# Kernel tuning notes

Measured on AMD Instinct MI355X. Metric: run time of the kernel, lower is better.

The kernel has to match this reference:

```python
import jax, jax.numpy as jnp
import numpy as np

LEAKY_SLOPE = 0.01  # torch F.leaky_relu default
COS_EPS = 1e-8      # torch F.cosine_similarity default eps


def _gc(pre, cur, adj, W):
    # GraphConvolution.forward
    pre_w = pre @ W            # [N, d]
    cur_w = cur @ W            # [M, d]
    new_pre = adj @ cur_w      # [N, d]
    new_cur = adj.T @ pre_w    # [M, d]
    new_pre = jnp.where(new_pre >= 0, new_pre, LEAKY_SLOPE * new_pre)
    new_cur = jnp.where(new_cur >= 0, new_cur, LEAKY_SLOPE * new_cur)
    return new_pre, new_cur


def _cos_sim(pre, cur):
    # Fused pairwise cosine similarity: matches torch F.cosine_similarity per pair
    dots = pre @ cur.T                         # [N, M]
    n_pre = jnp.linalg.norm(pre, axis=1)       # [N]
    n_cur = jnp.linalg.norm(cur, axis=1)       # [M]
    denom = jnp.maximum(n_pre[:, None] * n_cur[None, :], COS_EPS)
    return dots / denom


def setup_inputs() -> dict:
    key = jax.random.key(0)
    k1, k2, k3, k4, k5 = jax.random.split(key, 5)
    N, d = 8192, 128
    stdv = 1.0 / np.sqrt(d)
    pre = jax.random.normal(k1, (N, d), dtype=jnp.float32)
    cur = jax.random.normal(k2, (N, d), dtype=jnp.float32)
    adj = jax.random.uniform(k3, (N, N), dtype=jnp.float32)
    W1 = jax.random.uniform(k4, (d, d), dtype=jnp.float32, minval=-stdv, maxval=stdv)
    W2 = jax.random.uniform(k5, (d, d), dtype=jnp.float32, minval=-stdv, maxval=stdv)
    return {"pre": pre, "cur": cur, "adj": adj, "W1": W1, "W2": W2}


def reference(pre, cur, adj, W1, W2):
    pre1, cur1 = _gc(pre, cur, adj, W1)
    adj1 = _cos_sim(pre1, cur1)
    pre2, cur2 = _gc(pre1, cur1, adj1, W2)
    adj2 = _cos_sim(pre2, cur2)
    return adj2
```

## Files before the change

kernel.cpp:

```cpp
#include <hip/hip_runtime.h>


#define NN 8192
#define DD 128

typedef __bf16 bf16x8 __attribute__((ext_vector_type(8)));
typedef float f32x4 __attribute__((ext_vector_type(4)));

static __device__ __forceinline__ float4 ldg4(const float* p) {
    return *reinterpret_cast<const float4*>(p);
}

static __device__ __forceinline__ unsigned f2bf2(float lo, float hi) {
    __bf16 a = (__bf16)lo, b = (__bf16)hi;
    unsigned short ua = __builtin_bit_cast(unsigned short, a);
    unsigned short ub = __builtin_bit_cast(unsigned short, b);
    return (unsigned)ua | ((unsigned)ub << 16);
}

static __device__ __forceinline__ int swz16(int row) {
    return (((row & 7) ^ ((row >> 3) & 7)) << 4);
}

template<int AMODE>
__global__ __launch_bounds__(256, 2)
void mfma_tn(const void* __restrict__ Aptr, int lda,
             const unsigned short* __restrict__ BTa,
             const unsigned short* __restrict__ BTb, int ldbt,
             float* __restrict__ C, int ldc,
             int ksplit, int zstride)
{
    __shared__ uint4 smem4[2048];
    char* smem = (char*)smem4;
    char* smA = smem;
    char* smB = smem + 16384;

    const int t    = threadIdx.x;
    const int l    = t & 63;
    const int w    = t >> 6;
    const int wr   = (w >> 1) * 64;
    const int wc   = (w & 1) * 64;
    const int lrow = l & 15;
    const int lhi  = l >> 4;
    const int i0   = blockIdx.x * 128;
    const int j0   = blockIdx.y * 128;
    const int z    = blockIdx.z;
    const bool second = (AMODE == 3) && (z >= 8);
    const unsigned short* BT = second ? BTb : BTa;
    const int kbase = (AMODE == 3) ? (z & 7) * ksplit : 0;
    C += (size_t)z * (size_t)zstride;

    const int srow = t >> 3;
    const int skg  = t & 7;

    f32x4 acc[4][4];
    #pragma unroll
    for (int r = 0; r < 4; ++r)
        #pragma unroll
        for (int q = 0; q < 4; ++q)
            #pragma unroll
            for (int e = 0; e < 4; ++e) acc[r][q][e] = 0.0f;

    for (int k0 = 0; k0 < ksplit; k0 += 64) {
        const int kk = kbase + k0;

        if (AMODE == 3 && second) {
            const int u  = t & 31;
            const int r8 = t >> 5;
            const float* gA = (const float*)Aptr;
            float rv[8][4];
            #pragma unroll
            for (int e = 0; e < 8; ++e) {
                float4 v = ldg4(&gA[(size_t)(kk + r8 * 8 + e) * lda + i0 + u * 4]);
                rv[e][0] = v.x; rv[e][1] = v.y; rv[e][2] = v.z; rv[e][3] = v.w;
            }
            #pragma unroll
            for (int j = 0; j < 4; ++j) {
                const int c = u * 4 + j;
                uint4 wv;
                wv.x = f2bf2(rv[0][j], rv[1][j]);
                wv.y = f2bf2(rv[2][j], rv[3][j]);
                wv.z = f2bf2(rv[4][j], rv[5][j]);
                wv.w = f2bf2(rv[6][j], rv[7][j]);
                *reinterpret_cast<uint4*>(smA + c * 128 + ((r8 << 4) ^ swz16(c))) = wv;
            }
        } else {
            #pragma unroll
            for (int it = 0; it < 4; ++it) {
                const int row = it * 32 + srow;
                const int dst = row * 128 + ((skg << 4) ^ swz16(row));
                if constexpr (AMODE == 3) {
                    const float* g = (const float*)Aptr + (size_t)(i0 + row) * lda + kk + skg * 8;
                    float4 f0 = ldg4(g), f1 = ldg4(g + 4);
                    uint4 wv;
                    wv.x = f2bf2(f0.x, f0.y);
                    wv.y = f2bf2(f0.z, f0.w);
                    wv.z = f2bf2(f1.x, f1.y);
                    wv.w = f2bf2(f1.z, f1.w);
                    *reinterpret_cast<uint4*>(smA + dst) = wv;
                } else {
                    const unsigned short* g = (const unsigned short*)Aptr + (size_t)(i0 + row) * lda + kk + skg * 8;
                    *reinterpret_cast<uint4*>(smA + dst) = *reinterpret_cast<const uint4*>(g);
                }
            }
        }

        #pragma unroll
        for (int it = 0; it < 4; ++it) {
            const int row = it * 32 + srow;
            const int dst = row * 128 + ((skg << 4) ^ swz16(row));
            const unsigned short* gb = BT + (size_t)(j0 + row) * ldbt + kk + skg * 8;
            *reinterpret_cast<uint4*>(smB + dst) = *reinterpret_cast<const uint4*>(gb);
        }
        __syncthreads();

        #pragma unroll
        for (int s = 0; s < 2; ++s) {
            bf16x8 af[4], bq[4];
            #pragma unroll
            for (int r = 0; r < 4; ++r) {
                const int row = wr + r * 16 + lrow;
                af[r] = *reinterpret_cast<const bf16x8*>(
                    smA + row * 128 + ((s * 64 + lhi * 16) ^ swz16(row)));
            }
            #pragma unroll
            for (int q = 0; q < 4; ++q) {
                const int col = wc + q * 16 + lrow;
                bq[q] = *reinterpret_cast<const bf16x8*>(
                    smB + col * 128 + ((s * 64 + lhi * 16) ^ swz16(col)));
            }
            #pragma unroll
            for (int r = 0; r < 4; ++r)
                #pragma unroll
                for (int q = 0; q < 4; ++q)
                    acc[r][q] = __builtin_amdgcn_mfma_f32_16x16x32_bf16(af[r], bq[q], acc[r][q], 0, 0, 0);
        }
        __syncthreads();
    }

    float* sC = (float*)smem;
    #pragma unroll
    for (int h = 0; h < 2; ++h) {
        if ((w & 1) == h) {
            #pragma unroll
            for (int r = 0; r < 4; ++r)
                #pragma unroll
                for (int q = 0; q < 4; ++q)
                    #pragma unroll
                    for (int i = 0; i < 4; ++i)
                        sC[(wr + r * 16 + lhi * 4 + i) * 64 + q * 16 + lrow] = acc[r][q][i];
        }
        __syncthreads();
        #pragma unroll
        for (int it = 0; it < 8; ++it) {
            const int idx = it * 256 + t;
            const int row = idx >> 4;
            const int c4  = (idx & 15) << 2;
            float4 v = *reinterpret_cast<const float4*>(&sC[row * 64 + c4]);
            *reinterpret_cast<float4*>(&C[(size_t)(i0 + row) * ldc + j0 + h * 64 + c4]) = v;
        }
        __syncthreads();
    }
}

__global__ __launch_bounds__(256, 2)
void gemm_w1t(const float* __restrict__ pre, const float* __restrict__ cur,
              const float* __restrict__ W1,
              unsigned short* __restrict__ pwT, unsigned short* __restrict__ cwT)
{
    __shared__ float sA[32][68];
    __shared__ float sB[64][128];

    const int t  = threadIdx.x;
    const int ct = t & 31;
    const int rt = t >> 5;
    const int bx = blockIdx.x;
    const bool isCur = bx >= 256;
    const float* A = isCur ? cur : pre;
    unsigned short* XT = isCur ? cwT : pwT;
    const int i0 = (bx & 255) * 32;

    float4 acc[4];
    #pragma unroll
    for (int r = 0; r < 4; ++r) { acc[r].x = 0.f; acc[r].y = 0.f; acc[r].z = 0.f; acc[r].w = 0.f; }

    for (int k0 = 0; k0 < DD; k0 += 64) {
        #pragma unroll
        for (int f = 0; f < 2; ++f) {
            const int row = (t >> 4) + 16 * f;
            const int kk4 = (t & 15) << 2;
            *reinterpret_cast<float4*>(&sA[row][kk4]) =
                ldg4(&A[(size_t)(i0 + row) * DD + k0 + kk4]);
        }
        #pragma unroll
        for (int f = 0; f < 8; ++f) {
            const int idx = f * 256 + t;
            const int kk  = idx >> 5;
            const int c4  = (idx & 31) << 2;
            *reinterpret_cast<float4*>(&sB[kk][c4]) =
                ldg4(&W1[(size_t)(k0 + kk) * DD + c4]);
        }
        __syncthreads();
        #pragma unroll 4
        for (int kk = 0; kk < 64; kk += 4) {
            float4 a[4], b[4];
            #pragma unroll
            for (int r = 0; r < 4; ++r)
                a[r] = *reinterpret_cast<const float4*>(&sA[rt * 4 + r][kk]);
            #pragma unroll
            for (int q = 0; q < 4; ++q)
                b[q] = *reinterpret_cast<const float4*>(&sB[kk + q][ct * 4]);
            #pragma unroll
            for (int r = 0; r < 4; ++r) {
                acc[r].x += a[r].x * b[0].x; acc[r].y += a[r].x * b[0].y;
                acc[r].z += a[r].x * b[0].z; acc[r].w += a[r].x * b[0].w;
                acc[r].x += a[r].y * b[1].x; acc[r].y += a[r].y * b[1].y;
                acc[r].z += a[r].y * b[1].z; acc[r].w += a[r].y * b[1].w;
                acc[r].x += a[r].z * b[2].x; acc[r].y += a[r].z * b[2].y;
                acc[r].z += a[r].z * b[2].z; acc[r].w += a[r].z * b[2].w;
                acc[r].x += a[r].w * b[3].x; acc[r].y += a[r].w * b[3].y;
                acc[r].z += a[r].w * b[3].z; acc[r].w += a[r].w * b[3].w;
            }
        }
        __syncthreads();
    }

    float* sC = &sB[0][0];
    #pragma unroll
    for (int r = 0; r < 4; ++r)
        *reinterpret_cast<float4*>(&sC[(rt * 4 + r) * 128 + ct * 4]) = acc[r];
    __syncthreads();

    const int n = t & 127;
    const int g = t >> 7;
    #pragma unroll
    for (int c = 0; c < 2; ++c) {
        const int ii = (2 * g + c) * 8;
        uint4 wv;
        wv.x = f2bf2(sC[(ii + 0) * 128 + n], sC[(ii + 1) * 128 + n]);
        wv.y = f2bf2(sC[(ii + 2) * 128 + n], sC[(ii + 3) * 128 + n]);
        wv.z = f2bf2(sC[(ii + 4) * 128 + n], sC[(ii + 5) * 128 + n]);
        wv.w = f2bf2(sC[(ii + 6) * 128 + n], sC[(ii + 7) * 128 + n]);
        *reinterpret_cast<uint4*>(&XT[(size_t)n * NN + i0 + ii]) = wv;
    }
}

__global__ __launch_bounds__(128)
void rln(const float* __restrict__ kparts, float* __restrict__ Xbase,
         float* __restrict__ invbase)
{
    const int i = blockIdx.x;
    const int y = blockIdx.y;
    const int t = threadIdx.x;
    const float* part = kparts + (size_t)(1 - y) * 8 * (NN * DD);
    float* X = Xbase + (size_t)y * (NN * DD);
    float* inv_n = invbase + y * NN;

    float s = 0.f;
    #pragma unroll
    for (int z = 0; z < 8; ++z)
        s += part[(size_t)z * (NN * DD) + (size_t)i * DD + t];
    float y_ = (s >= 0.f) ? s : 0.01f * s;
    X[(size_t)i * DD + t] = y_;
    float n = y_ * y_;
    #pragma unroll
    for (int o = 32; o > 0; o >>= 1) n += __shfl_down(n, o);
    __shared__ float p[2];
    if ((t & 63) == 0) p[t >> 6] = n;
    __syncthreads();
    if (t == 0) inv_n[i] = 1.0f / sqrtf(p[0] + p[1]);
}

template<bool TRANSA, bool SCALEK, int EPI>
__global__ __launch_bounds__(256, 2)
void gemm32(const float* __restrict__ A, int lda,
            const float* __restrict__ B, int ldb,
            float* __restrict__ C, unsigned short* __restrict__ Cb,
            int ksplit_len, int zstride,
            const float* __restrict__ kscale,
            const float* __restrict__ rscale,
            int ystA, int ystB, int ystC, int ystS)
{
    __shared__ float sA[32][68];
    __shared__ float sB[64][128];

    const int t  = threadIdx.x;
    const int ct = t & 31;
    const int rt = t >> 5;
    const int i0 = blockIdx.x * 32;
    const int side = blockIdx.y;
    const int kgbase = blockIdx.z * ksplit_len;

    A += (ptrdiff_t)side * ystA;
    B += (ptrdiff_t)side * ystB;
    if constexpr (EPI == 0)
        C += (ptrdiff_t)side * ystC + (size_t)blockIdx.z * (size_t)zstride;
    if constexpr (EPI == 3)
        Cb += (ptrdiff_t)side * ystC;
    if constexpr (SCALEK) kscale += (ptrdiff_t)side * ystS;
    if constexpr (EPI == 3) rscale += (ptrdiff_t)side * ystS;

    float4 acc[4];
    #pragma unroll
    for (int r = 0; r < 4; ++r) { acc[r].x = 0.f; acc[r].y = 0.f; acc[r].z = 0.f; acc[r].w = 0.f; }

    for (int k0 = 0; k0 < ksplit_len; k0 += 64) {
        const int kg = kgbase + k0;
        if (!TRANSA) {
            #pragma unroll
            for (int f = 0; f < 2; ++f) {
                const int row = (t >> 4) + 16 * f;
                const int kk4 = (t & 15) << 2;
                *reinterpret_cast<float4*>(&sA[row][kk4]) =
                    ldg4(&A[(size_t)(i0 + row) * lda + kg + kk4]);
            }
        } else {
            #pragma unroll
            for (int f = 0; f < 2; ++f) {
                const int kk = (t >> 3) + 32 * f;
                const int r4 = (t & 7) << 2;
                float4 v = ldg4(&A[(size_t)(kg + kk) * lda + i0 + r4]);
                if (SCALEK) {
                    const float s = kscale[kg + kk];
                    v.x *= s; v.y *= s; v.z *= s; v.w *= s;
                }
                sA[r4 + 0][kk] = v.x; sA[r4 + 1][kk] = v.y;
                sA[r4 + 2][kk] = v.z; sA[r4 + 3][kk] = v.w;
            }
        }
        #pragma unroll
        for (int f = 0; f < 8; ++f) {
            const int idx = f * 256 + t;
            const int kk  = idx >> 5;
            const int c4  = (idx & 31) << 2;
            *reinterpret_cast<float4*>(&sB[kk][c4]) =
                ldg4(&B[(size_t)(kg + kk) * ldb + c4]);
        }
        __syncthreads();
        #pragma unroll 4
        for (int kk = 0; kk < 64; kk += 4) {
            float4 a[4], b[4];
            #pragma unroll
            for (int r = 0; r < 4; ++r)
                a[r] = *reinterpret_cast<const float4*>(&sA[rt * 4 + r][kk]);
            #pragma unroll
            for (int q = 0; q < 4; ++q)
                b[q] = *reinterpret_cast<const float4*>(&sB[kk + q][ct * 4]);
            #pragma unroll
            for (int r = 0; r < 4; ++r) {
                acc[r].x += a[r].x * b[0].x; acc[r].y += a[r].x * b[0].y;
                acc[r].z += a[r].x * b[0].z; acc[r].w += a[r].x * b[0].w;
                acc[r].x += a[r].y * b[1].x; acc[r].y += a[r].y * b[1].y;
                acc[r].z += a[r].y * b[1].z; acc[r].w += a[r].y * b[1].w;
                acc[r].x += a[r].z * b[2].x; acc[r].y += a[r].z * b[2].y;
                acc[r].z += a[r].z * b[2].z; acc[r].w += a[r].z * b[2].w;
                acc[r].x += a[r].w * b[3].x; acc[r].y += a[r].w * b[3].y;
                acc[r].z += a[r].w * b[3].z; acc[r].w += a[r].w * b[3].w;
            }
        }
        __syncthreads();
    }

    #pragma unroll
    for (int r = 0; r < 4; ++r) {
        const int rg = i0 + rt * 4 + r;
        if constexpr (EPI == 3) {
            const float s = rscale[rg];
            float y0 = acc[r].x * s, y1 = acc[r].y * s,
                  y2 = acc[r].z * s, y3 = acc[r].w * s;
            y0 = (y0 >= 0.f) ? y0 : 0.01f * y0;
            y1 = (y1 >= 0.f) ? y1 : 0.01f * y1;
            y2 = (y2 >= 0.f) ? y2 : 0.01f * y2;
            y3 = (y3 >= 0.f) ? y3 : 0.01f * y3;
            float ss = y0 * y0 + y1 * y1 + y2 * y2 + y3 * y3;
            #pragma unroll
            for (int m = 16; m > 0; m >>= 1) ss += __shfl_xor(ss, m);
            const float invn = rsqrtf(ss);
            uint2 wv;
            wv.x = f2bf2(y0 * invn, y1 * invn);
            wv.y = f2bf2(y2 * invn, y3 * invn);
            *reinterpret_cast<uint2*>(&Cb[(size_t)rg * DD + ct * 4]) = wv;
        } else {
            *reinterpret_cast<float4*>(&C[(size_t)rg * DD + ct * 4]) = acc[r];
        }
    }
}

__global__ __launch_bounds__(256)
void reduce_mcmp(const float* __restrict__ part, float* __restrict__ out)
{
    const int y = blockIdx.y;
    const int i = blockIdx.x * 256 + threadIdx.x;
    part += (size_t)y * 32 * 16384;
    out  += (size_t)y * 16384;
    float a = 0.f;
    #pragma unroll
    for (int z = 0; z < 32; ++z) a += part[(size_t)z * 16384 + i];
    out[i] = a;
}

extern "C" void kernel_launch(void* const* d_in, const int* in_sizes, int n_in,
                              void* d_out, int out_size, void* d_ws, size_t ws_size,
                              hipStream_t stream)
{
    const float* pre = (const float*)d_in[0];
    const float* cur = (const float*)d_in[1];
    const float* adj = (const float*)d_in[2];
    const float* W1  = (const float*)d_in[3];
    const float* W2  = (const float*)d_in[4];
    float* out = (float*)d_out;
    float* ws  = (float*)d_ws;

    const size_t M1 = (size_t)NN * DD;

    float* cwpw2 = ws + 0 * M1;
    float* c1    = ws + 2 * M1;
    unsigned short* c2n_b = (unsigned short*)(ws + 4 * M1);
    unsigned short* p2n_b = c2n_b + M1;
    unsigned short* cwT_b = (unsigned short*)(ws + 5 * M1);
    unsigned short* pwT_b = cwT_b + M1;
    float* bparts = ws + 6 * M1;
    float* mcmp   = ws + 7 * M1;
    float* inc1   = mcmp + 32768;
    float* kparts = ws + 8 * M1;

    gemm_w1t<<<dim3(512,1,1),256,0,stream>>>(pre, cur, W1, pwT_b, cwT_b);

    mfma_tn<3><<<dim3(64,1,16),256,0,stream>>>(adj, NN, cwT_b, pwT_b, NN,
                                               kparts, DD, NN/8, (int)M1);

    rln<<<dim3(NN,2,1),128,0,stream>>>(kparts, c1, inc1);

    gemm32<false,false,0><<<dim3(512,1,1),256,0,stream>>>(
        c1, DD, W2, DD, cwpw2, (unsigned short*)nullptr,
        DD, 0, nullptr, nullptr, 0,0,0,0);

    gemm32<true,true,0><<<dim3(4,2,32),256,0,stream>>>(
        c1, DD, cwpw2, DD, bparts, (unsigned short*)nullptr,
        256, 16384, inc1, nullptr,
        (int)M1, (int)M1, 32*16384, NN);

    reduce_mcmp<<<dim3(64,2,1),256,0,stream>>>(bparts, mcmp);

    gemm32<false,false,3><<<dim3(256,2,1),256,0,stream>>>(
        c1, DD, mcmp + 16384, DD, (float*)nullptr, c2n_b,
        DD, 0, nullptr, inc1,
        (int)M1, -16384, (int)M1, NN);

    mfma_tn<0><<<dim3(64,64,1),256,0,stream>>>(p2n_b, DD, c2n_b, c2n_b, DD,
                                               out, NN, DD, 0);
}
```

Measured before the change: 286.7 us.

## Double-buffer mfma_tn shared memory with register prefetch and halve split-K

The bf16 MFMA GEMM kernel now loads the next K-tile from global memory into registers while it runs MFMAs on the current tile, using two shared-memory buffers and one barrier per iteration. The split-K factor for the first adjacency GEMM drops from 8 to 4, which halves the partial buffers written and summed by rln. The epilogue pads the staging stride to 68 to avoid LDS bank conflicts and uses nontemporal stores for AMODE 0. Shared memory doubles to 64KB per block and register pressure rises, which may limit occupancy, and the grid shrinks to 512 blocks.

```diff
diff --git a/kernel.cpp b/kernel.cpp
--- a/kernel.cpp
+++ b/kernel.cpp
@@ -17,6 +17,8 @@
     unsigned short ub = __builtin_bit_cast(unsigned short, b);
     return (unsigned)ua | ((unsigned)ub << 16);
 }
+
+#define FCOMP(v, j) ((j) == 0 ? (v).x : (j) == 1 ? (v).y : (j) == 2 ? (v).z : (v).w)
 
 static __device__ __forceinline__ int swz16(int row) {
     return (((row & 7) ^ ((row >> 3) & 7)) << 4);
@@ -30,10 +32,8 @@
              float* __restrict__ C, int ldc,
              int ksplit, int zstride)
 {
-    __shared__ uint4 smem4[2048];
+    __shared__ uint4 smem4[4096];
     char* smem = (char*)smem4;
-    char* smA = smem;
-    char* smB = smem + 16384;
 
     const int t    = threadIdx.x;
     const int l    = t & 63;
@@ -45,13 +45,15 @@
     const int i0   = blockIdx.x * 128;
     const int j0   = blockIdx.y * 128;
     const int z    = blockIdx.z;
-    const bool second = (AMODE == 3) && (z >= 8);
+    const bool second = (AMODE == 3) && (z >= 4);
     const unsigned short* BT = second ? BTb : BTa;
-    const int kbase = (AMODE == 3) ? (z & 7) * ksplit : 0;
+    const int kbase = (AMODE == 3) ? (z & 3) * ksplit : 0;
     C += (size_t)z * (size_t)zstride;
 
     const int srow = t >> 3;
     const int skg  = t & 7;
+    const int u    = t & 31;
+    const int r8   = t >> 5;
 
     f32x4 acc[4][4];
     #pragma unroll
@@ -61,59 +63,79 @@
             #pragma unroll
             for (int e = 0; e < 4; ++e) acc[r][q][e] = 0.0f;
 
-    for (int k0 = 0; k0 < ksplit; k0 += 64) {
-        const int kk = kbase + k0;
-
+    float4 fa[8];
+    uint4  ua[4];
+    uint4  ub[4];
+
+    auto LOAD = [&](int kk) {
         if (AMODE == 3 && second) {
-            const int u  = t & 31;
-            const int r8 = t >> 5;
             const float* gA = (const float*)Aptr;
-            float rv[8][4];
-            #pragma unroll
-            for (int e = 0; e < 8; ++e) {
-                float4 v = ldg4(&gA[(size_t)(kk + r8 * 8 + e) * lda + i0 + u * 4]);
-                rv[e][0] = v.x; rv[e][1] = v.y; rv[e][2] = v.z; rv[e][3] = v.w;
-            }
+            #pragma unroll
+            for (int e = 0; e < 8; ++e)
+                fa[e] = ldg4(&gA[(size_t)(kk + r8 * 8 + e) * lda + i0 + u * 4]);
+        } else if (AMODE == 3) {
+            #pragma unroll
+            for (int it = 0; it < 4; ++it) {
+                const float* g = (const float*)Aptr + (size_t)(i0 + it * 32 + srow) * lda + kk + skg * 8;
+                fa[2 * it]     = ldg4(g);
+                fa[2 * it + 1] = ldg4(g + 4);
+            }
+        } else {
+            #pragma unroll
+            for (int it = 0; it < 4; ++it) {
+                const unsigned short* g = (const unsigned short*)Aptr + (size_t)(i0 + it * 32 + srow) * lda + kk + skg * 8;
+                ua[it] = *reinterpret_cast<const uint4*>(g);
+            }
+        }
+        #pragma unroll
+        for (int it = 0; it < 4; ++it) {
+            const unsigned short* gb = BT + (size_t)(j0 + it * 32 + srow) * ldbt + kk + skg * 8;
+            ub[it] = *reinterpret_cast<const uint4*>(gb);
+        }
+    };
+
+    auto WRITE = [&](int buf) {
+        char* smA = smem + buf * 32768;
+        char* smB = smA + 16384;
+        if (AMODE == 3 && second) {
             #pragma unroll
             for (int j = 0; j < 4; ++j) {
                 const int c = u * 4 + j;
                 uint4 wv;
-                wv.x = f2bf2(rv[0][j], rv[1][j]);
-                wv.y = f2bf2(rv[2][j], rv[3][j]);
-                wv.z = f2bf2(rv[4][j], rv[5][j]);
-                wv.w = f2bf2(rv[6][j], rv[7][j]);
+                wv.x = f2bf2(FCOMP(fa[0], j), FCOMP(fa[1], j));
+                wv.y = f2bf2(FCOMP(fa[2], j), FCOMP(fa[3], j));
+                wv.z = f2bf2(FCOMP(fa[4], j), FCOMP(fa[5], j));
+                wv.w = f2bf2(FCOMP(fa[6], j), FCOMP(fa[7], j));
                 *reinterpret_cast<uint4*>(smA + c * 128 + ((r8 << 4) ^ swz16(c))) = wv;
             }
-        } else {
+        } else if (AMODE == 3) {
             #pragma unroll
             for (int it = 0; it < 4; ++it) {
                 const int row = it * 32 + srow;
-                const int dst = row * 128 + ((skg << 4) ^ swz16(row));
-                if constexpr (AMODE == 3) {
-                    const float* g = (const float*)Aptr + (size_t)(i0 + row) * lda + kk + skg * 8;
-                    float4 f0 = ldg4(g), f1 = ldg4(g + 4);
-                    uint4 wv;
-                    wv.x = f2bf2(f0.x, f0.y);
-                    wv.y = f2bf2(f0.z, f0.w);
-                    wv.z = f2bf2(f1.x, f1.y);
-                    wv.w = f2bf2(f1.z, f1.w);
-                    *reinterpret_cast<uint4*>(smA + dst) = wv;
-                } else {
-                    const unsigned short* g = (const unsigned short*)Aptr + (size_t)(i0 + row) * lda + kk + skg * 8;
-                    *reinterpret_cast<uint4*>(smA + dst) = *reinterpret_cast<const uint4*>(g);
-                }
-            }
-        }
-
+                uint4 wv;
+                wv.x = f2bf2(fa[2 * it].x, fa[2 * it].y);
+                wv.y = f2bf2(fa[2 * it].z, fa[2 * it].w);
+                wv.z = f2bf2(fa[2 * it + 1].x, fa[2 * it + 1].y);
+                wv.w = f2bf2(fa[2 * it + 1].z, fa[2 * it + 1].w);
+                *reinterpret_cast<uint4*>(smA + row * 128 + ((skg << 4) ^ swz16(row))) = wv;
+            }
+        } else {
+            #pragma unroll
+            for (int it = 0; it < 4; ++it) {
+                const int row = it * 32 + srow;
+                *reinterpret_cast<uint4*>(smA + row * 128 + ((skg << 4) ^ swz16(row))) = ua[it];
+            }
+        }
         #pragma unroll
         for (int it = 0; it < 4; ++it) {
             const int row = it * 32 + srow;
-            const int dst = row * 128 + ((skg << 4) ^ swz16(row));
-            const unsigned short* gb = BT + (size_t)(j0 + row) * ldbt + kk + skg * 8;
-            *reinterpret_cast<uint4*>(smB + dst) = *reinterpret_cast<const uint4*>(gb);
-        }
-        __syncthreads();
-
+            *reinterpret_cast<uint4*>(smB + row * 128 + ((skg << 4) ^ swz16(row))) = ub[it];
+        }
+    };
+
+    auto MFMA_STEP = [&](int buf) {
+        char* smA = smem + buf * 32768;
+        char* smB = smA + 16384;
         #pragma unroll
         for (int s = 0; s < 2; ++s) {
             bf16x8 af[4], bq[4];
@@ -135,6 +157,17 @@
                 for (int q = 0; q < 4; ++q)
                     acc[r][q] = __builtin_amdgcn_mfma_f32_16x16x32_bf16(af[r], bq[q], acc[r][q], 0, 0, 0);
         }
+    };
+
+    const int nt = ksplit >> 6;
+    LOAD(kbase);
+    WRITE(0);
+    __syncthreads();
+    for (int tt = 0; tt < nt; ++tt) {
+        const int cur = tt & 1;
+        if (tt + 1 < nt) LOAD(kbase + (tt + 1) * 64);
+        MFMA_STEP(cur);
+        if (tt + 1 < nt) WRITE(cur ^ 1);
         __syncthreads();
     }
 
@@ -148,7 +181,7 @@
                 for (int q = 0; q < 4; ++q)
                     #pragma unroll
                     for (int i = 0; i < 4; ++i)
-                        sC[(wr + r * 16 + lhi * 4 + i) * 64 + q * 16 + lrow] = acc[r][q][i];
+                        sC[(wr + r * 16 + lhi * 4 + i) * 68 + q * 16 + lrow] = acc[r][q][i];
         }
         __syncthreads();
         #pragma unroll
@@ -156,8 +189,12 @@
             const int idx = it * 256 + t;
             const int row = idx >> 4;
             const int c4  = (idx & 15) << 2;
-            float4 v = *reinterpret_cast<const float4*>(&sC[row * 64 + c4]);
-            *reinterpret_cast<float4*>(&C[(size_t)(i0 + row) * ldc + j0 + h * 64 + c4]) = v;
+            f32x4 v = *reinterpret_cast<const f32x4*>(&sC[row * 68 + c4]);
+            float* dst = &C[(size_t)(i0 + row) * ldc + j0 + h * 64 + c4];
+            if constexpr (AMODE == 0)
+                __builtin_nontemporal_store(v, reinterpret_cast<f32x4*>(dst));
+            else
+                *reinterpret_cast<f32x4*>(dst) = v;
         }
         __syncthreads();
     }
@@ -252,13 +289,13 @@
     const int i = blockIdx.x;
     const int y = blockIdx.y;
     const int t = threadIdx.x;
-    const float* part = kparts + (size_t)(1 - y) * 8 * (NN * DD);
+    const float* part = kparts + (size_t)(1 - y) * 4 * (NN * DD);
     float* X = Xbase + (size_t)y * (NN * DD);
     float* inv_n = invbase + y * NN;
 
     float s = 0.f;
     #pragma unroll
-    for (int z = 0; z < 8; ++z)
+    for (int z = 0; z < 4; ++z)
         s += part[(size_t)z * (NN * DD) + (size_t)i * DD + t];
     float y_ = (s >= 0.f) ? s : 0.01f * s;
     X[(size_t)i * DD + t] = y_;
@@ -426,8 +463,8 @@
 
     gemm_w1t<<<dim3(512,1,1),256,0,stream>>>(pre, cur, W1, pwT_b, cwT_b);
 
-    mfma_tn<3><<<dim3(64,1,16),256,0,stream>>>(adj, NN, cwT_b, pwT_b, NN,
-                                               kparts, DD, NN/8, (int)M1);
+    mfma_tn<3><<<dim3(64,1,8),256,0,stream>>>(adj, NN, cwT_b, pwT_b, NN,
+                                              kparts, DD, NN/4, (int)M1);
 
     rln<<<dim3(NN,2,1),128,0,stream>>>(kparts, c1, inc1);
 
```

Result: slower. 294.2 us (+2.6%).

## Split MFMA GEMM into adj and output kernels with 128-deep K tiles

Applied to the files above, without the earlier changes.

Replaces the templated mfma_tn kernel with two specialised kernels. mfma_adj stages 128-wide K chunks per iteration (64KB LDS), halving the number of barriers per K and issuing more loads in flight. mfma_out loads the full K=128 panel once with a single sync and writes the accumulators straight to global memory instead of staging them through LDS. The larger LDS footprint may limit occupancy to one block per CU despite launch_bounds(256,2), and the direct output stores are less coalesced.

```diff
diff --git a/kernel.cpp b/kernel.cpp
--- a/kernel.cpp
+++ b/kernel.cpp
@@ -18,22 +18,154 @@
     return (unsigned)ua | ((unsigned)ub << 16);
 }
 
+#define FC(v, j) ((j) == 0 ? (v).x : (j) == 1 ? (v).y : (j) == 2 ? (v).z : (v).w)
+
+#define PRAGU _Pragma("unroll")
+
 static __device__ __forceinline__ int swz16(int row) {
     return (((row & 7) ^ ((row >> 3) & 7)) << 4);
 }
-
-template<int AMODE>
+static __device__ __forceinline__ int lslot(int row, int slot) {
+    return ((slot & 8) << 4) | (((slot & 7) << 4) ^ swz16(row));
+}
+
 __global__ __launch_bounds__(256, 2)
-void mfma_tn(const void* __restrict__ Aptr, int lda,
-             const unsigned short* __restrict__ BTa,
-             const unsigned short* __restrict__ BTb, int ldbt,
-             float* __restrict__ C, int ldc,
-             int ksplit, int zstride)
-{
-    __shared__ uint4 smem4[2048];
-    char* smem = (char*)smem4;
+void mfma_adj(const float* __restrict__ adj,
+              const unsigned short* __restrict__ BTa,
+              const unsigned short* __restrict__ BTb,
+              float* __restrict__ C, int ksplit, int zstride)
+{
+    __shared__ alignas(16) char smem[65536];
     char* smA = smem;
-    char* smB = smem + 16384;
+    char* smB = smem + 32768;
+
+    const int t    = threadIdx.x;
+    const int l    = t & 63;
+    const int w    = t >> 6;
+    const int wr   = (w >> 1) * 64;
+    const int wc   = (w & 1) * 64;
+    const int lrow = l & 15;
+    const int lhi  = l >> 4;
+    const int i0   = blockIdx.x * 128;
+    const int z    = blockIdx.z;
+    const bool second = z >= 8;
+    const unsigned short* BT = second ? BTb : BTa;
+    const int kbase = (z & 7) * ksplit;
+    C += (size_t)z * (size_t)zstride;
+
+    const int srow = t >> 3;
+    const int skg  = t & 7;
+    const int u    = t & 31;
+    const int r8   = t >> 5;
+
+    f32x4 acc[4][4];
+    PRAGU
+    for (int r = 0; r < 4; ++r)
+        PRAGU
+        for (int q = 0; q < 4; ++q)
+            PRAGU
+            for (int e = 0; e < 4; ++e) acc[r][q][e] = 0.0f;
+
+    const int nt = ksplit >> 7;
+    for (int tc = 0; tc < nt; ++tc) {
+        const int kk = kbase + tc * 128;
+
+        PRAGU
+        for (int h = 0; h < 2; ++h) {
+            const int kh = kk + h * 64;
+            if (second) {
+                float4 rv[8];
+                PRAGU
+                for (int e = 0; e < 8; ++e)
+                    rv[e] = ldg4(&adj[(size_t)(kh + r8 * 8 + e) * NN + i0 + u * 4]);
+                PRAGU
+                for (int j = 0; j < 4; ++j) {
+                    const int c = u * 4 + j;
+                    uint4 wv;
+                    wv.x = f2bf2(FC(rv[0], j), FC(rv[1], j));
+                    wv.y = f2bf2(FC(rv[2], j), FC(rv[3], j));
+                    wv.z = f2bf2(FC(rv[4], j), FC(rv[5], j));
+                    wv.w = f2bf2(FC(rv[6], j), FC(rv[7], j));
+                    *reinterpret_cast<uint4*>(smA + c * 256 + lslot(c, h * 8 + r8)) = wv;
+                }
+            } else {
+                PRAGU
+                for (int it = 0; it < 4; ++it) {
+                    const int row = it * 32 + srow;
+                    const float* g = adj + (size_t)(i0 + row) * NN + kh + skg * 8;
+                    float4 f0 = ldg4(g), f1 = ldg4(g + 4);
+                    uint4 wv;
+                    wv.x = f2bf2(f0.x, f0.y);
+                    wv.y = f2bf2(f0.z, f0.w);
+                    wv.z = f2bf2(f1.x, f1.y);
+                    wv.w = f2bf2(f1.z, f1.w);
+                    *reinterpret_cast<uint4*>(smA + row * 256 + lslot(row, h * 8 + skg)) = wv;
+                }
+            }
+            PRAGU
+            for (int it = 0; it < 4; ++it) {
+                const int n = it * 32 + srow;
+                *reinterpret_cast<uint4*>(smB + n * 256 + lslot(n, h * 8 + skg)) =
+                    *reinterpret_cast<const uint4*>(BT + (size_t)n * NN + kh + skg * 8);
+            }
+        }
+        __syncthreads();
+
+        PRAGU
+        for (int s = 0; s < 4; ++s) {
+            bf16x8 af[4], bq[4];
+            PRAGU
+            for (int r = 0; r < 4; ++r) {
+                const int row = wr + r * 16 + lrow;
+                af[r] = *reinterpret_cast<const bf16x8*>(smA + row * 256 + lslot(row, s * 4 + lhi));
+            }
+            PRAGU
+            for (int q = 0; q < 4; ++q) {
+                const int col = wc + q * 16 + lrow;
+                bq[q] = *reinterpret_cast<const bf16x8*>(smB + col * 256 + lslot(col, s * 4 + lhi));
+            }
+            PRAGU
+            for (int r = 0; r < 4; ++r)
+                PRAGU
+                for (int q = 0; q < 4; ++q)
+                    acc[r][q] = __builtin_amdgcn_mfma_f32_16x16x32_bf16(af[r], bq[q], acc[r][q], 0, 0, 0);
+        }
+        __syncthreads();
+    }
+
+    float* sC = (float*)smem;
+    PRAGU
+    for (int h = 0; h < 2; ++h) {
+        if ((w & 1) == h) {
+            PRAGU
+            for (int r = 0; r < 4; ++r)
+                PRAGU
+                for (int q = 0; q < 4; ++q)
+                    PRAGU
+                    for (int i = 0; i < 4; ++i)
+                        sC[(wr + r * 16 + lhi * 4 + i) * 68 + q * 16 + lrow] = acc[r][q][i];
+        }
+        __syncthreads();
+        PRAGU
+        for (int it = 0; it < 8; ++it) {
+            const int idx = it * 256 + t;
+            const int row = idx >> 4;
+            const int c4  = (idx & 15) << 2;
+            f32x4 v = *reinterpret_cast<const f32x4*>(&sC[row * 68 + c4]);
+            *reinterpret_cast<f32x4*>(&C[(size_t)(i0 + row) * DD + h * 64 + c4]) = v;
+        }
+        __syncthreads();
+    }
+}
+
+__global__ __launch_bounds__(256, 2)
+void mfma_out(const unsigned short* __restrict__ A,
+              const unsigned short* __restrict__ BT,
+              float* __restrict__ C)
+{
+    __shared__ alignas(16) char smem[65536];
+    char* smA = smem;
+    char* smB = smem + 32768;
 
     const int t    = threadIdx.x;
     const int l    = t & 63;
@@ -44,123 +176,57 @@
     const int lhi  = l >> 4;
     const int i0   = blockIdx.x * 128;
     const int j0   = blockIdx.y * 128;
-    const int z    = blockIdx.z;
-    const bool second = (AMODE == 3) && (z >= 8);
-    const unsigned short* BT = second ? BTb : BTa;
-    const int kbase = (AMODE == 3) ? (z & 7) * ksplit : 0;
-    C += (size_t)z * (size_t)zstride;
-
-    const int srow = t >> 3;
-    const int skg  = t & 7;
+    const int s16  = t >> 4;
+    const int slot = t & 15;
 
     f32x4 acc[4][4];
-    #pragma unroll
+    PRAGU
     for (int r = 0; r < 4; ++r)
-        #pragma unroll
+        PRAGU
         for (int q = 0; q < 4; ++q)
-            #pragma unroll
+            PRAGU
             for (int e = 0; e < 4; ++e) acc[r][q][e] = 0.0f;
 
-    for (int k0 = 0; k0 < ksplit; k0 += 64) {
-        const int kk = kbase + k0;
-
-        if (AMODE == 3 && second) {
-            const int u  = t & 31;
-            const int r8 = t >> 5;
-            const float* gA = (const float*)Aptr;
-            float rv[8][4];
-            #pragma unroll
-            for (int e = 0; e < 8; ++e) {
-                float4 v = ldg4(&gA[(size_t)(kk + r8 * 8 + e) * lda + i0 + u * 4]);
-                rv[e][0] = v.x; rv[e][1] = v.y; rv[e][2] = v.z; rv[e][3] = v.w;
-            }
-            #pragma unroll
-            for (int j = 0; j < 4; ++j) {
-                const int c = u * 4 + j;
-                uint4 wv;
-                wv.x = f2bf2(rv[0][j], rv[1][j]);
-                wv.y = f2bf2(rv[2][j], rv[3][j]);
-                wv.z = f2bf2(rv[4][j], rv[5][j]);
-                wv.w = f2bf2(rv[6][j], rv[7][j]);
-                *reinterpret_cast<uint4*>(smA + c * 128 + ((r8 << 4) ^ swz16(c))) = wv;
-            }
-        } else {
-            #pragma unroll
-            for (int it = 0; it < 4; ++it) {
-                const int row = it * 32 + srow;
-                const int dst = row * 128 + ((skg << 4) ^ swz16(row));
-                if constexpr (AMODE == 3) {
-                    const float* g = (const float*)Aptr + (size_t)(i0 + row) * lda + kk + skg * 8;
-                    float4 f0 = ldg4(g), f1 = ldg4(g + 4);
-                    uint4 wv;
-                    wv.x = f2bf2(f0.x, f0.y);
-                    wv.y = f2bf2(f0.z, f0.w);
-                    wv.z = f2bf2(f1.x, f1.y);
-                    wv.w = f2bf2(f1.z, f1.w);
-                    *reinterpret_cast<uint4*>(smA + dst) = wv;
-                } else {
-                    const unsigned short* g = (const unsigned short*)Aptr + (size_t)(i0 + row) * lda + kk + skg * 8;
-                    *reinterpret_cast<uint4*>(smA + dst) = *reinterpret_cast<const uint4*>(g);
-                }
-            }
-        }
-
-        #pragma unroll
-        for (int it = 0; it < 4; ++it) {
-            const int row = it * 32 + srow;
-            const int dst = row * 128 + ((skg << 4) ^ swz16(row));
-            const unsigned short* gb = BT + (size_t)(j0 + row) * ldbt + kk + skg * 8;
-            *reinterpret_cast<uint4*>(smB + dst) = *reinterpret_cast<const uint4*>(gb);
-        }
-        __syncthreads();
-
-        #pragma unroll
-        for (int s = 0; s < 2; ++s) {
-            bf16x8 af[4], bq[4];
-            #pragma unroll
-            for (int r = 0; r < 4; ++r) {
-                const int row = wr + r * 16 + lrow;
-                af[r] = *reinterpret_cast<const bf16x8*>(
-                    smA + row * 128 + ((s * 64 + lhi * 16) ^ swz16(row)));
-            }
-            #pragma unroll
-            for (int q = 0; q < 4; ++q) {
-                const int col = wc + q * 16 + lrow;
-                bq[q] = *reinterpret_cast<const bf16x8*>(
-                    smB + col * 128 + ((s * 64 + lhi * 16) ^ swz16(col)));
-            }
-            #pragma unroll
-            for (int r = 0; r < 4; ++r)
-                #pragma unroll
-                for (int q = 0; q < 4; ++q)
-                    acc[r][q] = __builtin_amdgcn_mfma_f32_16x16x32_bf16(af[r], bq[q], acc[r][q], 0, 0, 0);
-        }
-        __syncthreads();
-    }
-
-    float* sC = (float*)smem;
-    #pragma unroll
-    for (int h = 0; h < 2; ++h) {
-        if ((w & 1) == h) {
-            #pragma unroll
-            for (int r = 0; r < 4; ++r)
-                #pragma unroll
-                for (int q = 0; q < 4; ++q)
-                    #pragma unroll
-                    for (int i = 0; i < 4; ++i)
-                        sC[(wr + r * 16 + lhi * 4 + i) * 64 + q * 16 + lrow] = acc[r][q][i];
-        }
-        __syncthreads();
-        #pragma unroll
-        for (int it = 0; it < 8; ++it) {
-            const int idx = it * 256 + t;
-            const int row = idx >> 4;
-            const int c4  = (idx & 15) << 2;
-            float4 v = *reinterpret_cast<const float4*>(&sC[row * 64 + c4]);
-            *reinterpret_cast<float4*>(&C[(size_t)(i0 + row) * ldc + j0 + h * 64 + c4]) = v;
-        }
-        __syncthreads();
-    }
+    PRAGU
+    for (int it = 0; it < 8; ++it) {
+        const int row = it * 16 + s16;
+        *reinterpret_cast<uint4*>(smA + row * 256 + lslot(row, slot)) =
+            *reinterpret_cast<const uint4*>(A + (size_t)(i0 + row) * DD + slot * 8);
+        *reinterpret_cast<uint4*>(smB + row * 256 + lslot(row, slot)) =
+            *reinterpret_cast<const uint4*>(BT + (size_t)(j0 + row) * DD + slot * 8);
+    }
+    __syncthreads();
+
+    PRAGU
+    for (int s = 0; s < 4; ++s) {
+        bf16x8 af[4], bq[4];
+        PRAGU
+        for (int r = 0; r < 4; ++r) {
+            const int row = wr + r * 16 + lrow;
+            af[r] = *reinterpret_cast<const bf16x8*>(smA + row * 256 + lslot(row, s * 4 + lhi));
+        }
+        PRAGU
+        for (int q = 0; q < 4; ++q) {
+            const int col = wc + q * 16 + lrow;
+            bq[q] = *reinterpret_cast<const bf16x8*>(smB + col * 256 + lslot(col, s * 4 + lhi));
+        }
+        PRAGU
+        for (int r = 0; r < 4; ++r)
+            PRAGU
+            for (int q = 0; q < 4; ++q)
+                acc[r][q] = __builtin_amdgcn_mfma_f32_16x16x32_bf16(af[r], bq[q], acc[r][q], 0, 0, 0);
+    }
+
+    PRAGU
+    for (int r = 0; r < 4; ++r)
+        PRAGU
+        for (int i = 0; i < 4; ++i) {
+            const int grow = i0 + wr + r * 16 + lhi * 4 + i;
+            float* cp = C + (size_t)grow * NN + j0 + wc;
+            PRAGU
+            for (int q = 0; q < 4; ++q)
+                cp[q * 16 + lrow] = acc[r][q][i];
+        }
 }
 
 __global__ __launch_bounds__(256, 2)
@@ -426,8 +492,8 @@
 
     gemm_w1t<<<dim3(512,1,1),256,0,stream>>>(pre, cur, W1, pwT_b, cwT_b);
 
-    mfma_tn<3><<<dim3(64,1,16),256,0,stream>>>(adj, NN, cwT_b, pwT_b, NN,
-                                               kparts, DD, NN/8, (int)M1);
+    mfma_adj<<<dim3(64,1,16),256,0,stream>>>(adj, cwT_b, pwT_b,
+                                             kparts, NN/8, (int)M1);
 
     rln<<<dim3(NN,2,1),128,0,stream>>>(kparts, c1, inc1);
 
@@ -447,6 +513,5 @@
         DD, 0, nullptr, inc1,
         (int)M1, -16384, (int)M1, NN);
 
-    mfma_tn<0><<<dim3(64,64,1),256,0,stream>>>(p2n_b, DD, c2n_b, c2n_b, DD,
-                                               out, NN, DD, 0);
-}
+    mfma_out<<<dim3(64,64,1),256,0,stream>>>(p2n_b, c2n_b, out);
+}
```

Result: slower. 300.3 us (+4.7%).
